# Performance work log

Measured on AMD Instinct MI355X. Metric: run time of the kernel, lower is better.

## Reference

```python
import jax, jax.numpy as jnp
import numpy as np

E, H, G = 1024, 16, 1          # embed_dim, num_heads, gqa_factor
HKV = H // G                   # kv heads
D = E // H                     # head_dim
EKV = HKV * D                  # kv_embed_dim
B, TQ, TK = 4, 512, 1024
CLAMP = float(-np.log(1.0 / 0.98 - 1.0))  # neg_prob_to_phi(clamp_prob=0.98)
SCALE = float(1.0 / np.sqrt(D))           # 1/norm_fact
NEG = -1e30                                # ~ -inf in log space


def monotonic_attention(phi):
    """Log-space monotonic alignment DP over the last axis.
    phi: (N, Ti, Tj) clamped transition logits. Returns log alignment probs, same shape.
    alpha[i,0] = 0 if i==0 else -inf
    alpha[i,j] = logaddexp(alpha[i,j-1] + logsigmoid(phi[i,j-1]),      # stay at row i
                           alpha[i-1,j-1] + logsigmoid(-phi[i-1,j-1])) # advance to row i
    """
    log_p = jax.nn.log_sigmoid(phi)
    log_1mp = jax.nn.log_sigmoid(-phi)
    N, Ti, Tj = phi.shape
    alpha0 = jnp.full((N, Ti), NEG, phi.dtype).at[:, 0].set(0.0)
    neg_col = jnp.full((N, 1), NEG, phi.dtype)

    def step(alpha, cols):
        lp, l1mp = cols  # each (N, Ti)
        stay = alpha + lp
        move = jnp.concatenate([neg_col, (alpha + l1mp)[:, :-1]], axis=1)
        new = jnp.logaddexp(stay, move)
        return new, new

    xs = (jnp.moveaxis(log_p[:, :, :-1], -1, 0), jnp.moveaxis(log_1mp[:, :, :-1], -1, 0))
    _, rest = jax.lax.scan(step, alpha0, xs)             # (Tj-1, N, Ti)
    alphas = jnp.concatenate([alpha0[None], rest], axis=0)  # (Tj, N, Ti)
    return jnp.moveaxis(alphas, 0, -1)                   # (N, Ti, Tj)


def setup_inputs() -> dict:
    k = jax.random.key(0)
    ks = jax.random.split(k, 5)
    bw = float(np.sqrt(6.0 / ((2 * E + 2 * EKV) + E)))  # xavier_uniform bound
    bo = float(1.0 / np.sqrt(E))                        # nn.Linear default bound
    return {
        "query": jax.random.normal(ks[0], (B, TQ, E), jnp.float32),
        "key": jax.random.normal(ks[1], (B, TK, E), jnp.float32),
        "value": jax.random.normal(ks[2], (B, TK, E), jnp.float32),
        "in_proj_weight": jax.random.uniform(ks[3], (2 * E + 2 * EKV, E), jnp.float32, -bw, bw),
        "in_proj_bias": jnp.zeros((2 * E + 2 * EKV,), jnp.float32),
        "out_w": jax.random.uniform(ks[4], (E, E), jnp.float32, -bo, bo),
        "out_b": jnp.zeros((E,), jnp.float32),
    }


def reference(query, key, value, in_proj_weight, in_proj_bias, out_w, out_b):
    qwa, qw, kw, vw = jnp.split(in_proj_weight, [E, 2 * E, 2 * E + EKV], axis=0)
    qba, qb, kb, vb = jnp.split(in_proj_bias, [E, 2 * E, 2 * E + EKV])

    def proj(x, w, b, g):
        y = x @ w.T + b
        Bx, T, _ = x.shape
        return y.reshape(Bx, T, g, HKV, D).transpose(0, 2, 3, 1, 4)  # (B,g,HKV,T,D)

    xqa = proj(query, qwa, qba, G)  # monotonic query
    xq = proj(query, qw, qb, G)     # regular query
    xk = proj(key, kw, kb, 1)
    xv = proj(value, vw, vb, 1)

    # mode = 'many_keys_one_query': DP grid has key rows, query cols
    phi = jnp.einsum('bghqc,bghkc->bghkq', xqa, xk)
    phi = jnp.tanh(phi) * CLAMP  # soft clamp
    mono = monotonic_attention(phi.reshape(-1, TK, TQ)).reshape(B, G, HKV, TK, TQ)
    mono = jnp.swapaxes(mono, -2, -1)  # (B,G,H,TQ,TK)

    reg = jnp.einsum('bghqc,bghkc->bghqk', xq, xk) * SCALE
    attn = jax.nn.softmax(reg + mono, axis=-1)
    xo = jnp.einsum('bghqk,bghkc->bghqc', attn, xv)
    xo = xo.transpose(0, 3, 1, 2, 4).reshape(B, TQ, E)
    return xo @ out_w.T + out_b
```

## Files before the change

kernel.cpp:

```cpp
#include <hip/hip_runtime.h>
#include <hip/hip_fp16.h>
#include <hip/hip_bf16.h>
#include <math.h>

typedef unsigned short u16;
typedef __attribute__((ext_vector_type(8))) short bf16x8;
typedef __attribute__((ext_vector_type(8))) unsigned short u16x8;
typedef __attribute__((ext_vector_type(4))) unsigned short u16x4;
typedef __attribute__((ext_vector_type(4))) float f32x4;

static constexpr float CLAMPF = 3.8918202981106265f;
static constexpr float SCALEF = 0.125f;
static constexpr float ASCALE = 16384.f;

__device__ __forceinline__ u16 f2bf(float x) {
    __hip_bfloat16 h = __float2bfloat16(x);
    return *reinterpret_cast<u16*>(&h);
}

__global__ __launch_bounds__(256)
void cvt_all_k(const float* __restrict__ q, const float* __restrict__ key,
               const float* __restrict__ val, const float* __restrict__ W,
               const float* __restrict__ ow,
               u16* __restrict__ QBF, u16* __restrict__ KBF,
               u16* __restrict__ VBF, u16* __restrict__ WBF,
               u16* __restrict__ OWBF)
{
    long i = (long)blockIdx.x * 256 + threadIdx.x;
    float4 v;
    u16* dst; long off;
    if (i < 524288) {
        dst = QBF; off = i;
        v = ((const float4*)q)[i];
    } else if (i < 1048576) {
        off = i - 524288;
        long r = off >> 8, c4 = off & 255;
        long b = r >> 9, tok = r & 511;
        dst = KBF;
        v = ((const float4*)key)[(b * 1024 + tok) * 256 + c4];
    } else if (i < 1572864) {
        off = i - 1048576;
        long r = off >> 8, c4 = off & 255;
        long b = r >> 9, tok = r & 511;
        dst = VBF;
        v = ((const float4*)val)[(b * 1024 + tok) * 256 + c4];
    } else if (i < 2621440) {
        dst = WBF; off = i - 1572864;
        v = ((const float4*)W)[off];
    } else if (i < 2883584) {
        dst = OWBF; off = i - 2621440;
        v = ((const float4*)ow)[off];
    } else return;
    u16x4 o; o.x = f2bf(v.x); o.y = f2bf(v.y); o.z = f2bf(v.z); o.w = f2bf(v.w);
    ((u16x4*)dst)[off] = o;
}

template<int TM, int TN, int EPI, bool TRI>
__device__ __forceinline__
void mfma_body(u16* As, u16* Bs, int bx, int by, int bz,
               const u16* __restrict__ Ag, const u16* __restrict__ Bg,
               void* __restrict__ Cg, const float* __restrict__ bias,
               int K, int lda, int ldb, int ldc,
               long sAb, long sAh, long sBb, long sBh, long sCb, long sCh,
               int hdiv)
{
    int b = bz / hdiv, h = bz % hdiv;
    const u16* A = Ag + (long)b * sAb + (long)h * sAh;
    const u16* B = Bg + (long)b * sBb + (long)h * sBh;

    int tid = threadIdx.x;
    int bm = by * TM, bn = bx * TN;

    constexpr int AC = TM / 32;
    constexpr int BC = TN / 32;
    int srow = tid >> 3;
    int scol = (tid & 7) * 8;

    int wid = tid >> 6, lane = tid & 63;
    int wr = wid >> 1, wc = wid & 1;
    constexpr int MI = TM / 32;
    constexpr int NI = TN / 32;
    int arow0 = wr * (TM / 2) + (lane & 15);
    int bcol0 = wc * (TN / 2) + (lane & 15);
    int koff = (lane >> 4) * 8;

    if constexpr (TRI) {
        if (bx > by) {
            __half* C = (__half*)Cg + (long)b * sCb + (long)h * sCh;
            int rb = bm + wr * (TM / 2) + (lane >> 4) * 4;
            int cb = bn + wc * (TN / 2) + (lane & 15);
            __half z16 = __float2half(0.f);
#pragma unroll
            for (int mi = 0; mi < MI; ++mi)
#pragma unroll
                for (int ni = 0; ni < NI; ++ni)
#pragma unroll
                    for (int r = 0; r < 4; ++r)
                        C[(long)(rb + 16 * mi + r) * ldc + cb + 16 * ni] = z16;
            return;
        }
    }

    f32x4 acc[MI][NI];
#pragma unroll
    for (int i = 0; i < MI; ++i)
#pragma unroll
        for (int j = 0; j < NI; ++j) acc[i][j] = (f32x4){0.f, 0.f, 0.f, 0.f};

    for (int kt = 0; kt < K; kt += 64) {
        u16x8 av[AC], bv[BC];
#pragma unroll
        for (int c = 0; c < AC; ++c)
            av[c] = *(const u16x8*)(A + (long)(bm + srow + 32 * c) * lda + kt + scol);
#pragma unroll
        for (int c = 0; c < BC; ++c)
            bv[c] = *(const u16x8*)(B + (long)(bn + srow + 32 * c) * ldb + kt + scol);
        __syncthreads();
#pragma unroll
        for (int c = 0; c < AC; ++c)
            *(u16x8*)&As[(srow + 32 * c) * 64 + scol] = av[c];
#pragma unroll
        for (int c = 0; c < BC; ++c)
            *(u16x8*)&Bs[(srow + 32 * c) * 64 + scol] = bv[c];
        __syncthreads();

#pragma unroll
        for (int ks = 0; ks < 2; ++ks) {
            bf16x8 af[MI], bfr[NI];
#pragma unroll
            for (int mi = 0; mi < MI; ++mi)
                af[mi] = *(const bf16x8*)&As[(arow0 + 16 * mi) * 64 + ks * 32 + koff];
#pragma unroll
            for (int ni = 0; ni < NI; ++ni)
                bfr[ni] = *(const bf16x8*)&Bs[(bcol0 + 16 * ni) * 64 + ks * 32 + koff];
#pragma unroll
            for (int mi = 0; mi < MI; ++mi)
#pragma unroll
                for (int ni = 0; ni < NI; ++ni)
                    acc[mi][ni] = __builtin_amdgcn_mfma_f32_16x16x32_bf16(
                        af[mi], bfr[ni], acc[mi][ni], 0, 0, 0);
        }
    }

    int rbase = bm + wr * (TM / 2) + (lane >> 4) * 4;
    int cbase = bn + wc * (TN / 2) + (lane & 15);
#pragma unroll
    for (int mi = 0; mi < MI; ++mi) {
#pragma unroll
        for (int ni = 0; ni < NI; ++ni) {
            int m0 = rbase + 16 * mi;
            int n = cbase + 16 * ni;
            if constexpr (EPI == 0) {
                u16* C = (u16*)Cg + (long)b * sCb + (long)h * sCh;
                float bvv = bias ? bias[n] : 0.f;
#pragma unroll
                for (int r = 0; r < 4; ++r)
                    C[(long)(m0 + r) * ldc + n] = f2bf(acc[mi][ni][r] + bvv);
            } else if constexpr (EPI == 1) {
                __half* C = (__half*)Cg + (long)b * sCb + (long)h * sCh;
#pragma unroll
                for (int r = 0; r < 4; ++r) {
                    float x = acc[mi][ni][r];
                    float e2 = __expf(2.f * x);
                    float tv = CLAMPF - (2.f * CLAMPF) * __builtin_amdgcn_rcpf(e2 + 1.f);
                    float pv = __builtin_amdgcn_rcpf(1.f + __expf(-tv));
                    C[(long)(m0 + r) * ldc + n] = __float2half(pv);
                }
            } else if constexpr (EPI == 3) {
                float* C = (float*)Cg + (long)b * sCb + (long)h * sCh;
                float bvv = bias[n];
#pragma unroll
                for (int r = 0; r < 4; ++r)
                    C[(long)(m0 + r) * ldc + n] = acc[mi][ni][r] + bvv;
            } else {
                u16* C = (u16*)Cg;
                float bvv = bias[n];
                long vaddr = ((long)(b * 16 + (n >> 6)) * 64 + (n & 63)) * 512 + m0;
                u16x4 pk;
                pk.x = f2bf(acc[mi][ni][0] + bvv);
                pk.y = f2bf(acc[mi][ni][1] + bvv);
                pk.z = f2bf(acc[mi][ni][2] + bvv);
                pk.w = f2bf(acc[mi][ni][3] + bvv);
                *(u16x4*)(C + vaddr) = pk;
            }
        }
    }
}

template<int TM, int TN, int EPI, bool TRI = false>
__global__ __launch_bounds__(256)
void mfma_nt(const u16* __restrict__ Ag, const u16* __restrict__ Bg,
             void* __restrict__ Cg, const float* __restrict__ bias,
             int K, int lda, int ldb, int ldc,
             long sAb, long sAh, long sBb, long sBh, long sCb, long sCh,
             int hdiv)
{
    __shared__ u16 As[TM * 64];
    __shared__ u16 Bs[TN * 64];
    mfma_body<TM, TN, EPI, TRI>(As, Bs, blockIdx.x, blockIdx.y, blockIdx.z,
                                Ag, Bg, Cg, bias, K, lda, ldb, ldc,
                                sAb, sAh, sBb, sBh, sCb, sCh, hdiv);
}

__global__ __launch_bounds__(256)
void proj_qk_k(const u16* __restrict__ QBF, const u16* __restrict__ KBF,
               const u16* __restrict__ WBF, const float* __restrict__ ipb,
               u16* __restrict__ XQAQ, u16* __restrict__ XK)
{
    __shared__ u16 As[128 * 64];
    __shared__ u16 Bs[128 * 64];
    int bid = blockIdx.x;
    if (bid < 128) {
        mfma_body<128, 128, 0, false>(As, Bs, bid & 7, bid >> 3, 0,
            QBF, WBF, XQAQ, ipb, 1024, 1024, 1024, 2048, 0, 0, 0, 0, 0, 0, 1);
    } else {
        int idx = bid - 128;
        mfma_body<128, 128, 0, false>(As, Bs, idx & 7, (idx >> 3) & 3, idx >> 5,
            KBF, WBF + 2097152, XK, ipb + 2048, 1024, 1024, 1024, 1024,
            524288L, 0, 0, 0, 524288L, 0, 1);
    }
}


__global__ __launch_bounds__(64)
void dpA_k(const __half* __restrict__ P, __half* __restrict__ BND)
{
    int g = blockIdx.x;
    int n = blockIdx.y;
    int lane = threadIdx.x;
    const __half* p = P + (long)n * 262144;
    int k0 = lane * 8;

    float band[8][9];
#pragma unroll
    for (int r = 0; r < 8; ++r)
#pragma unroll
        for (int d = 0; d < 9; ++d) band[r][d] = 0.f;

    {
        uint4 pc4 = *(const uint4*)(p + (long)(8 * g) * 512 + k0);
        const __half2* hp = (const __half2*)&pc4;
        float pc[8];
        { float2 t = __half22float2(hp[0]); pc[0] = t.x; pc[1] = t.y; }
        { float2 t = __half22float2(hp[1]); pc[2] = t.x; pc[3] = t.y; }
        { float2 t = __half22float2(hp[2]); pc[4] = t.x; pc[5] = t.y; }
        { float2 t = __half22float2(hp[3]); pc[6] = t.x; pc[7] = t.y; }
        float p7s = __shfl_up(pc[7], 1, 64);
#pragma unroll
        for (int r = 0; r < 8; ++r) band[r][0] = pc[r];
        band[0][1] = (lane == 0) ? 0.f : (1.f - p7s);
#pragma unroll
        for (int r = 1; r < 8; ++r) band[r][1] = 1.f - pc[r - 1];
    }

    for (int s = 1; s < 8; ++s) {
        uint4 pc4 = *(const uint4*)(p + (long)(8 * g + s) * 512 + k0);
        const __half2* hp = (const __half2*)&pc4;
        float pc[8];
        { float2 t = __half22float2(hp[0]); pc[0] = t.x; pc[1] = t.y; }
        { float2 t = __half22float2(hp[1]); pc[2] = t.x; pc[3] = t.y; }
        { float2 t = __half22float2(hp[2]); pc[4] = t.x; pc[5] = t.y; }
        { float2 t = __half22float2(hp[3]); pc[6] = t.x; pc[7] = t.y; }
        float p7s = __shfl_up(pc[7], 1, 64);
        float qm0 = (lane == 0) ? 0.f : (1.f - p7s);
        float qm[8];
        qm[0] = qm0;
#pragma unroll
        for (int r = 1; r < 8; ++r) qm[r] = 1.f - pc[r - 1];
        float prev7[9];
#pragma unroll
        for (int d = 0; d < 9; ++d) {
            float v = __shfl_up(band[7][d], 1, 64);
            prev7[d] = (lane == 0) ? 0.f : v;
        }
#pragma unroll
        for (int r = 7; r >= 1; --r) {
#pragma unroll
            for (int d = 8; d >= 1; --d)
                band[r][d] = fmaf(qm[r], band[r - 1][d - 1], pc[r] * band[r][d]);
            band[r][0] = pc[r] * band[r][0];
        }
#pragma unroll
        for (int d = 8; d >= 1; --d)
            band[0][d] = fmaf(qm0, prev7[d - 1], pc[0] * band[0][d]);
        band[0][0] = pc[0] * band[0][0];
    }

    long gb = (long)(n * 63 + g) * 9 * 512;
#pragma unroll
    for (int d = 0; d < 9; ++d) {
        uint4 st;
        __half2 h0 = __floats2half2_rn(band[0][d], band[1][d]);
        __half2 h1 = __floats2half2_rn(band[2][d], band[3][d]);
        __half2 h2 = __floats2half2_rn(band[4][d], band[5][d]);
        __half2 h3 = __floats2half2_rn(band[6][d], band[7][d]);
        st.x = *(unsigned*)&h0; st.y = *(unsigned*)&h1;
        st.z = *(unsigned*)&h2; st.w = *(unsigned*)&h3;
        *(uint4*)(BND + gb + (long)d * 512 + k0) = st;
    }
}

__global__ __launch_bounds__(256)
void dpB_misc_k(const __half* __restrict__ BND, float* __restrict__ BSTATE,
                const u16* __restrict__ QBF, const u16* __restrict__ VBF,
                const u16* __restrict__ WBF, const float* __restrict__ ipb,
                u16* __restrict__ XQAQ, u16* __restrict__ VT)
{
    __shared__ u16 As[128 * 64];
    __shared__ u16 Bs[128 * 64];
    int bid = blockIdx.x;

    if (bid >= 192) {
        int idx = bid - 192;
        mfma_body<128, 128, 0, false>(As, Bs, 8 + (idx & 7), idx >> 3, 0,
            QBF, WBF, XQAQ, ipb, 1024, 1024, 1024, 2048, 0, 0, 0, 0, 0, 0, 1);
        return;
    }
    if (bid >= 64) {
        int idx = bid - 64;
        mfma_body<128, 128, 4, false>(As, Bs, idx & 7, (idx >> 3) & 3, idx >> 5,
            VBF, WBF + 3145728, VT, ipb + 3072, 1024, 1024, 1024, 0,
            524288L, 0, 0, 0, 0, 0, 1);
        return;
    }

    if (threadIdx.x >= 64) return;
    int n = bid;
    int lane = threadIdx.x;
    int k0 = lane * 8;
    const __half* bnd = BND + (long)n * 63 * 9 * 512;
    float* bst = BSTATE + (long)n * 64 * 512;

    float b[8];
#pragma unroll
    for (int r = 0; r < 8; ++r) b[r] = 0.f;
    if (lane == 0) b[0] = ASCALE;
    {
        float4 v0; v0.x = b[0]; v0.y = b[1]; v0.z = b[2]; v0.w = b[3];
        float4 v1; v1.x = b[4]; v1.y = b[5]; v1.z = b[6]; v1.w = b[7];
        *(float4*)(bst + k0) = v0;
        *(float4*)(bst + k0 + 4) = v1;
    }

    uint4 cur[9], nxt[9];
#pragma unroll
    for (int d = 0; d < 9; ++d)
        cur[d] = *(const uint4*)(bnd + (long)d * 512 + k0);

    for (int g = 0; g < 63; ++g) {
        if (g + 1 < 63) {
#pragma unroll
            for (int d = 0; d < 9; ++d)
                nxt[d] = *(const uint4*)(bnd + ((long)(g + 1) * 9 + d) * 512 + k0);
        }
        float pb[8];
#pragma unroll
        for (int r = 0; r < 8; ++r) {
            float v = __shfl_up(b[r], 1, 64);
            pb[r] = (lane == 0) ? 0.f : v;
        }
        float bn[8];
#pragma unroll
        for (int r = 0; r < 8; ++r) bn[r] = 0.f;
#pragma unroll
        for (int d = 0; d < 9; ++d) {
            const __half2* hp = (const __half2*)&cur[d];
            float f[8];
            { float2 t = __half22float2(hp[0]); f[0] = t.x; f[1] = t.y; }
            { float2 t = __half22float2(hp[1]); f[2] = t.x; f[3] = t.y; }
            { float2 t = __half22float2(hp[2]); f[4] = t.x; f[5] = t.y; }
            { float2 t = __half22float2(hp[3]); f[6] = t.x; f[7] = t.y; }
#pragma unroll
            for (int r = 0; r < 8; ++r) {
                float src = (r - d >= 0) ? b[r - d] : pb[8 + r - d];
                bn[r] = fmaf(f[r], src, bn[r]);
            }
        }
#pragma unroll
        for (int r = 0; r < 8; ++r) b[r] = bn[r];
        {
            float4 v0; v0.x = b[0]; v0.y = b[1]; v0.z = b[2]; v0.w = b[3];
            float4 v1; v1.x = b[4]; v1.y = b[5]; v1.z = b[6]; v1.w = b[7];
            *(float4*)(bst + (long)(g + 1) * 512 + k0) = v0;
            *(float4*)(bst + (long)(g + 1) * 512 + k0 + 4) = v1;
        }
#pragma unroll
        for (int d = 0; d < 9; ++d) cur[d] = nxt[d];
    }
}

#define CSTEP(PC, J) do { \
    const __half2* hp = (const __half2*)&(PC); \
    float pv[8]; \
    { float2 t = __half22float2(hp[0]); pv[0] = t.x; pv[1] = t.y; } \
    { float2 t = __half22float2(hp[1]); pv[2] = t.x; pv[3] = t.y; } \
    { float2 t = __half22float2(hp[2]); pv[4] = t.x; pv[5] = t.y; } \
    { float2 t = __half22float2(hp[3]); pv[6] = t.x; pv[7] = t.y; } \
    float c[8]; \
    _Pragma("unroll") \
    for (int r = 0; r < 8; ++r) c[r] = fmaf(-a[r], pv[r], a[r]); \
    float cp = __shfl_up(c[7], 1, 64); \
    if (lane == 0) cp = 0.f; \
    a[0] = fmaf(a[0], pv[0], cp); \
    _Pragma("unroll") \
    for (int r = 1; r < 8; ++r) a[r] = fmaf(a[r], pv[r], c[r - 1]); \
    uint4 st; \
    { __half2 h0 = __floats2half2_rn(a[0], a[1]), h1 = __floats2half2_rn(a[2], a[3]); \
      st.x = *(unsigned*)&h0; st.y = *(unsigned*)&h1; } \
    { __half2 h2 = __floats2half2_rn(a[4], a[5]), h3 = __floats2half2_rn(a[6], a[7]); \
      st.z = *(unsigned*)&h2; st.w = *(unsigned*)&h3; } \
    *(uint4*)(al + (long)(J) * 512 + k0) = st; \
} while (0)

__global__ __launch_bounds__(64)
void dpC_k(const __half* __restrict__ P, const float* __restrict__ BSTATE,
           __half* __restrict__ AL)
{
    int g = blockIdx.x;
    int n = blockIdx.y;
    int lane = threadIdx.x;
    const __half* p = P + (long)n * 262144;
    __half* al = AL + (long)n * 262144;
    int k0 = lane * 8;
    const float* bst = BSTATE + ((long)n * 64 + g) * 512;

    float a[8];
    {
        float4 v0 = *(const float4*)(bst + k0);
        float4 v1 = *(const float4*)(bst + k0 + 4);
        a[0] = v0.x; a[1] = v0.y; a[2] = v0.z; a[3] = v0.w;
        a[4] = v1.x; a[5] = v1.y; a[6] = v1.z; a[7] = v1.w;
    }
    if (g == 0) {
        uint4 st;
        __half2 h0 = __floats2half2_rn(a[0], a[1]), h1 = __floats2half2_rn(a[2], a[3]);
        __half2 h2 = __floats2half2_rn(a[4], a[5]), h3 = __floats2half2_rn(a[6], a[7]);
        st.x = *(unsigned*)&h0; st.y = *(unsigned*)&h1;
        st.z = *(unsigned*)&h2; st.w = *(unsigned*)&h3;
        *(uint4*)(al + k0) = st;
    }

    int t0 = 8 * g + 1;
    int nt = 511 - 8 * g; if (nt > 8) nt = 8;

    uint4 f0 = *(const uint4*)(p + (long)min(8 * g + 0, 510) * 512 + k0);
    uint4 f1 = *(const uint4*)(p + (long)min(8 * g + 1, 510) * 512 + k0);
    uint4 f2 = *(const uint4*)(p + (long)min(8 * g + 2, 510) * 512 + k0);
    uint4 f3 = *(const uint4*)(p + (long)min(8 * g + 3, 510) * 512 + k0);
    uint4 f4 = *(const uint4*)(p + (long)min(8 * g + 4, 510) * 512 + k0);
    uint4 f5 = *(const uint4*)(p + (long)min(8 * g + 5, 510) * 512 + k0);
    uint4 f6 = *(const uint4*)(p + (long)min(8 * g + 6, 510) * 512 + k0);
    uint4 f7 = *(const uint4*)(p + (long)min(8 * g + 7, 510) * 512 + k0);

    CSTEP(f0, t0 + 0);
    CSTEP(f1, t0 + 1);
    CSTEP(f2, t0 + 2);
    CSTEP(f3, t0 + 3);
    CSTEP(f4, t0 + 4);
    CSTEP(f5, t0 + 5);
    CSTEP(f6, t0 + 6);
    if (nt == 8) CSTEP(f7, t0 + 7);
}

__global__ __launch_bounds__(256, 4)
void fused_attn_k(const u16* __restrict__ XQAQ, const u16* __restrict__ XK,
                  const u16* __restrict__ VT, const __half* __restrict__ AL,
                  u16* __restrict__ XO)
{
    __shared__ u16 wtile[4][2048];
    __shared__ float co[4][16][64];
    __shared__ float cml[4][2][16];

    int n = blockIdx.x; int b = n >> 4, h = n & 15;
    int tid = threadIdx.x, wave = tid >> 6, lane = tid & 63;
    int l15 = lane & 15, l4 = lane >> 4;
    int qg = blockIdx.y * 16;
    u16* wlds = wtile[wave];
    int swz = (l15 & 7) << 3;

    float m = -3.0e38f, lsum = 0.f;
    f32x4 o[4];
#pragma unroll
    for (int df = 0; df < 4; ++df) o[df] = (f32x4){0.f, 0.f, 0.f, 0.f};

    if (wave * 128 < qg + 16) {
        const u16* qbase = XQAQ + (long)(b * 512 + qg + l15) * 2048 + 1024 + h * 64 + l4 * 8;
        bf16x8 qf0 = *(const bf16x8*)(qbase);
        bf16x8 qf1 = *(const bf16x8*)(qbase + 32);

        const u16* kbase = XK + (long)(b * 512 + wave * 128 + l15) * 1024 + h * 64 + l4 * 8;
        const __half* abase = AL + (long)(n * 512 + qg + l15) * 512 + wave * 128 + l4 * 4;
        const u16* vbase = VT + (long)(n * 64 + l15) * 512 + wave * 128 + l4 * 8;

        uint2 areg[8];
#pragma unroll
        for (int kf = 0; kf < 8; ++kf)
            areg[kf] = *(const uint2*)(abase + kf * 16);

        f32x4 s[8];
#pragma unroll
        for (int kf = 0; kf < 8; ++kf) {
            const u16* kb = kbase + (long)(kf * 16) * 1024;
            bf16x8 k0 = *(const bf16x8*)kb;
            bf16x8 k1 = *(const bf16x8*)(kb + 32);
            f32x4 acc = (f32x4){0.f, 0.f, 0.f, 0.f};
            acc = __builtin_amdgcn_mfma_f32_16x16x32_bf16(k0, qf0, acc, 0, 0, 0);
            acc = __builtin_amdgcn_mfma_f32_16x16x32_bf16(k1, qf1, acc, 0, 0, 0);
            s[kf] = acc;
        }

        float mt = -3.0e38f;
#pragma unroll
        for (int kf = 0; kf < 8; ++kf)
            mt = fmaxf(mt, fmaxf(fmaxf(s[kf][0], s[kf][1]), fmaxf(s[kf][2], s[kf][3])));
        mt = fmaxf(mt, __shfl_xor(mt, 16, 64));
        mt = fmaxf(mt, __shfl_xor(mt, 32, 64));
        m = mt;
        float negm = -mt * SCALEF;

#pragma unroll
        for (int kf = 0; kf < 8; ++kf) {
            float2 a01 = __half22float2(*(__half2*)&areg[kf].x);
            float2 a23 = __half22float2(*(__half2*)&areg[kf].y);
            float w0 = a01.x * __expf(fmaf(s[kf][0], SCALEF, negm));
            float w1 = a01.y * __expf(fmaf(s[kf][1], SCALEF, negm));
            float w2 = a23.x * __expf(fmaf(s[kf][2], SCALEF, negm));
            float w3 = a23.y * __expf(fmaf(s[kf][3], SCALEF, negm));
            lsum += (w0 + w1) + (w2 + w3);
            u16x4 wp; wp.x = f2bf(w0); wp.y = f2bf(w1); wp.z = f2bf(w2); wp.w = f2bf(w3);
            *(u16x4*)&wlds[(l15 * 128 + kf * 16 + l4 * 4) ^ swz] = wp;
        }

#pragma unroll
        for (int ks2 = 0; ks2 < 4; ++ks2) {
            bf16x8 wf = *(const bf16x8*)&wlds[(l15 * 128 + ks2 * 32 + l4 * 8) ^ swz];
#pragma unroll
            for (int df = 0; df < 4; ++df) {
                const u16* vb = vbase + (long)(df * 16) * 512 + ks2 * 32;
                bf16x8 vf = *(const bf16x8*)vb;
                o[df] = __builtin_amdgcn_mfma_f32_16x16x32_bf16(wf, vf, o[df], 0, 0, 0);
            }
        }

        lsum += __shfl_xor(lsum, 16, 64);
        lsum += __shfl_xor(lsum, 32, 64);
    }

    if (lane < 16) { cml[wave][0][l15] = m; cml[wave][1][l15] = lsum; }
#pragma unroll
    for (int df = 0; df < 4; ++df)
#pragma unroll
        for (int r = 0; r < 4; ++r)
            co[wave][l4 * 4 + r][df * 16 + l15] = o[df][r];
    __syncthreads();

    int q = tid >> 4, d0 = (tid & 15) * 4;
    float m0 = cml[0][0][q], m1 = cml[1][0][q], m2 = cml[2][0][q], m3 = cml[3][0][q];
    float ms = fmaxf(fmaxf(m0, m1), fmaxf(m2, m3));
    float c0w = __expf((m0 - ms) * SCALEF), c1w = __expf((m1 - ms) * SCALEF);
    float c2w = __expf((m2 - ms) * SCALEF), c3w = __expf((m3 - ms) * SCALEF);
    float lt = c0w * cml[0][1][q] + c1w * cml[1][1][q]
             + c2w * cml[2][1][q] + c3w * cml[3][1][q];
    f32x4 o0 = *(const f32x4*)&co[0][q][d0];
    f32x4 o1 = *(const f32x4*)&co[1][q][d0];
    f32x4 o2 = *(const f32x4*)&co[2][q][d0];
    f32x4 o3 = *(const f32x4*)&co[3][q][d0];
    float inv = __builtin_amdgcn_rcpf(lt);
    u16x4 st;
#pragma unroll
    for (int j = 0; j < 4; ++j)
        st[j] = f2bf((c0w * o0[j] + c1w * o1[j] + c2w * o2[j] + c3w * o3[j]) * inv);
    *(u16x4*)&XO[(long)(b * 512 + qg + q) * 1024 + h * 64 + d0] = st;
}

extern "C" void kernel_launch(void* const* d_in, const int* in_sizes, int n_in,
                              void* d_out, int out_size, void* d_ws, size_t ws_size,
                              hipStream_t stream)
{
    const float* q   = (const float*)d_in[0];
    const float* key = (const float*)d_in[1];
    const float* val = (const float*)d_in[2];
    const float* W   = (const float*)d_in[3];
    const float* ipb = (const float*)d_in[4];
    const float* ow  = (const float*)d_in[5];
    const float* ob  = (const float*)d_in[6];
    float* out = (float*)d_out;
    char* w = (char*)d_ws;

    __half* PSIG   = (__half*)(w);
    u16*    XQAQ   = (u16*)(w + 33554432);
    u16*    XK     = (u16*)(w + 41943040);
    u16*    VT     = (u16*)(w + 46137344);
    u16*    XO     = (u16*)(w + 50331648);
    u16*    OWBF   = (u16*)(w + 54525952);
    u16*    KBF    = (u16*)(w + 56623104);
    u16*    VBF    = (u16*)(w + 60817408);
    u16*    WBF    = (u16*)(w + 65011712);
    float*  BSTATE = (float*)(w + 73400320);
    __half* ALPHA  = (__half*)(w + 81788928);
    __half* BND    = (__half*)(w + 81788928);
    u16*    QBF    = (u16*)(w + 50331648);

    dim3 blk(256);

    cvt_all_k<<<dim3(11264), blk, 0, stream>>>(
        q, key, val, W, ow, QBF, KBF, VBF, WBF, OWBF);

    proj_qk_k<<<dim3(256), blk, 0, stream>>>(QBF, KBF, WBF, ipb, XQAQ, XK);

    mfma_nt<128, 128, 1, true><<<dim3(4, 4, 64), blk, 0, stream>>>(
        XQAQ, XK, PSIG, nullptr, 64, 2048, 1024, 512,
        1048576L, 64, 524288L, 64, 4194304L, 262144L, 16);

    dpA_k<<<dim3(63, 64), dim3(64), 0, stream>>>(PSIG, BND);

    dpB_misc_k<<<dim3(320), blk, 0, stream>>>(
        BND, BSTATE, QBF, VBF, WBF, ipb, XQAQ, VT);

    dpC_k<<<dim3(64, 64), dim3(64), 0, stream>>>(PSIG, BSTATE, ALPHA);

    fused_attn_k<<<dim3(64, 32, 1), blk, 0, stream>>>(XQAQ, XK, VT, ALPHA, XO);

    mfma_nt<128, 128, 3><<<dim3(8, 16, 1), blk, 0, stream>>>(
        XO, OWBF, out, ob, 1024, 1024, 1024, 1024, 0, 0, 0, 0, 0, 0, 1);
}
```

Before: 175.2 us.

## Fuse DP column recompute into attention kernel and move GEMMs into dpA

```diff
diff --git a/kernel.cpp b/kernel.cpp
--- a/kernel.cpp
+++ b/kernel.cpp
@@ -222,12 +222,33 @@
 }
 
 
-__global__ __launch_bounds__(64)
-void dpA_k(const __half* __restrict__ P, __half* __restrict__ BND)
-{
-    int g = blockIdx.x;
-    int n = blockIdx.y;
-    int lane = threadIdx.x;
+__global__ __launch_bounds__(256)
+void dpA_k(const __half* __restrict__ P, __half* __restrict__ BND,
+           const u16* __restrict__ QBF, const u16* __restrict__ VBF,
+           const u16* __restrict__ WBF, const float* __restrict__ ipb,
+           u16* __restrict__ XQAQ, u16* __restrict__ VT)
+{
+    __shared__ u16 As[128 * 64];
+    __shared__ u16 Bs[128 * 64];
+    int bid = blockIdx.x;
+
+    if (bid >= 1136) {
+        int idx = bid - 1136;
+        mfma_body<128, 128, 0, false>(As, Bs, 8 + (idx & 7), idx >> 3, 0,
+            QBF, WBF, XQAQ, ipb, 1024, 1024, 1024, 2048, 0, 0, 0, 0, 0, 0, 1);
+        return;
+    }
+    if (bid >= 1008) {
+        int idx = bid - 1008;
+        mfma_body<128, 128, 4, false>(As, Bs, idx & 7, (idx >> 3) & 3, idx >> 5,
+            VBF, WBF + 3145728, VT, ipb + 3072, 1024, 1024, 1024, 0,
+            524288L, 0, 0, 0, 0, 0, 1);
+        return;
+    }
+
+    int wave = threadIdx.x >> 6, lane = threadIdx.x & 63;
+    int idx = bid * 4 + wave;
+    int g = idx % 63, n = idx / 63;
     const __half* p = P + (long)n * 262144;
     int k0 = lane * 8;
 
@@ -300,32 +321,10 @@
     }
 }
 
-__global__ __launch_bounds__(256)
-void dpB_misc_k(const __half* __restrict__ BND, float* __restrict__ BSTATE,
-                const u16* __restrict__ QBF, const u16* __restrict__ VBF,
-                const u16* __restrict__ WBF, const float* __restrict__ ipb,
-                u16* __restrict__ XQAQ, u16* __restrict__ VT)
-{
-    __shared__ u16 As[128 * 64];
-    __shared__ u16 Bs[128 * 64];
-    int bid = blockIdx.x;
-
-    if (bid >= 192) {
-        int idx = bid - 192;
-        mfma_body<128, 128, 0, false>(As, Bs, 8 + (idx & 7), idx >> 3, 0,
-            QBF, WBF, XQAQ, ipb, 1024, 1024, 1024, 2048, 0, 0, 0, 0, 0, 0, 1);
-        return;
-    }
-    if (bid >= 64) {
-        int idx = bid - 64;
-        mfma_body<128, 128, 4, false>(As, Bs, idx & 7, (idx >> 3) & 3, idx >> 5,
-            VBF, WBF + 3145728, VT, ipb + 3072, 1024, 1024, 1024, 0,
-            524288L, 0, 0, 0, 0, 0, 1);
-        return;
-    }
-
-    if (threadIdx.x >= 64) return;
-    int n = bid;
+__global__ __launch_bounds__(64)
+void dpB_k(const __half* __restrict__ BND, float* __restrict__ BSTATE)
+{
+    int n = blockIdx.x;
     int lane = threadIdx.x;
     int k0 = lane * 8;
     const __half* bnd = BND + (long)n * 63 * 9 * 512;
@@ -342,17 +341,20 @@
         *(float4*)(bst + k0 + 4) = v1;
     }
 
-    uint4 cur[9], nxt[9];
+    uint4 cur[9], nxt[9], nxt2[9];
 #pragma unroll
     for (int d = 0; d < 9; ++d)
         cur[d] = *(const uint4*)(bnd + (long)d * 512 + k0);
+#pragma unroll
+    for (int d = 0; d < 9; ++d)
+        nxt[d] = *(const uint4*)(bnd + ((long)min(1, 62) * 9 + d) * 512 + k0);
 
     for (int g = 0; g < 63; ++g) {
-        if (g + 1 < 63) {
-#pragma unroll
-            for (int d = 0; d < 9; ++d)
-                nxt[d] = *(const uint4*)(bnd + ((long)(g + 1) * 9 + d) * 512 + k0);
-        }
+        int gp = min(g + 2, 62);
+#pragma unroll
+        for (int d = 0; d < 9; ++d)
+            nxt2[d] = *(const uint4*)(bnd + ((long)gp * 9 + d) * 512 + k0);
+
         float pb[8];
 #pragma unroll
         for (int r = 0; r < 8; ++r) {
@@ -385,11 +387,11 @@
             *(float4*)(bst + (long)(g + 1) * 512 + k0 + 4) = v1;
         }
 #pragma unroll
-        for (int d = 0; d < 9; ++d) cur[d] = nxt[d];
-    }
-}
-
-#define CSTEP(PC, J) do { \
+        for (int d = 0; d < 9; ++d) { cur[d] = nxt[d]; nxt[d] = nxt2[d]; }
+    }
+}
+
+#define FSTEP(PC, ROW) do { \
     const __half2* hp = (const __half2*)&(PC); \
     float pv[8]; \
     { float2 t = __half22float2(hp[0]); pv[0] = t.x; pv[1] = t.y; } \
@@ -409,74 +411,67 @@
       st.x = *(unsigned*)&h0; st.y = *(unsigned*)&h1; } \
     { __half2 h2 = __floats2half2_rn(a[4], a[5]), h3 = __floats2half2_rn(a[6], a[7]); \
       st.z = *(unsigned*)&h2; st.w = *(unsigned*)&h3; } \
-    *(uint4*)(al + (long)(J) * 512 + k0) = st; \
+    *(uint4*)&alds[ROW][k0] = st; \
 } while (0)
 
-__global__ __launch_bounds__(64)
-void dpC_k(const __half* __restrict__ P, const float* __restrict__ BSTATE,
-           __half* __restrict__ AL)
-{
-    int g = blockIdx.x;
-    int n = blockIdx.y;
-    int lane = threadIdx.x;
-    const __half* p = P + (long)n * 262144;
-    __half* al = AL + (long)n * 262144;
-    int k0 = lane * 8;
-    const float* bst = BSTATE + ((long)n * 64 + g) * 512;
-
-    float a[8];
-    {
-        float4 v0 = *(const float4*)(bst + k0);
-        float4 v1 = *(const float4*)(bst + k0 + 4);
-        a[0] = v0.x; a[1] = v0.y; a[2] = v0.z; a[3] = v0.w;
-        a[4] = v1.x; a[5] = v1.y; a[6] = v1.z; a[7] = v1.w;
-    }
-    if (g == 0) {
-        uint4 st;
-        __half2 h0 = __floats2half2_rn(a[0], a[1]), h1 = __floats2half2_rn(a[2], a[3]);
-        __half2 h2 = __floats2half2_rn(a[4], a[5]), h3 = __floats2half2_rn(a[6], a[7]);
-        st.x = *(unsigned*)&h0; st.y = *(unsigned*)&h1;
-        st.z = *(unsigned*)&h2; st.w = *(unsigned*)&h3;
-        *(uint4*)(al + k0) = st;
-    }
-
-    int t0 = 8 * g + 1;
-    int nt = 511 - 8 * g; if (nt > 8) nt = 8;
-
-    uint4 f0 = *(const uint4*)(p + (long)min(8 * g + 0, 510) * 512 + k0);
-    uint4 f1 = *(const uint4*)(p + (long)min(8 * g + 1, 510) * 512 + k0);
-    uint4 f2 = *(const uint4*)(p + (long)min(8 * g + 2, 510) * 512 + k0);
-    uint4 f3 = *(const uint4*)(p + (long)min(8 * g + 3, 510) * 512 + k0);
-    uint4 f4 = *(const uint4*)(p + (long)min(8 * g + 4, 510) * 512 + k0);
-    uint4 f5 = *(const uint4*)(p + (long)min(8 * g + 5, 510) * 512 + k0);
-    uint4 f6 = *(const uint4*)(p + (long)min(8 * g + 6, 510) * 512 + k0);
-    uint4 f7 = *(const uint4*)(p + (long)min(8 * g + 7, 510) * 512 + k0);
-
-    CSTEP(f0, t0 + 0);
-    CSTEP(f1, t0 + 1);
-    CSTEP(f2, t0 + 2);
-    CSTEP(f3, t0 + 3);
-    CSTEP(f4, t0 + 4);
-    CSTEP(f5, t0 + 5);
-    CSTEP(f6, t0 + 6);
-    if (nt == 8) CSTEP(f7, t0 + 7);
-}
-
-__global__ __launch_bounds__(256, 4)
+__global__ __launch_bounds__(256)
 void fused_attn_k(const u16* __restrict__ XQAQ, const u16* __restrict__ XK,
-                  const u16* __restrict__ VT, const __half* __restrict__ AL,
-                  u16* __restrict__ XO)
+                  const u16* __restrict__ VT, const __half* __restrict__ P,
+                  const float* __restrict__ BSTATE, u16* __restrict__ XO)
 {
     __shared__ u16 wtile[4][2048];
     __shared__ float co[4][16][64];
     __shared__ float cml[4][2][16];
+    __shared__ __half alds[16][520];
 
     int n = blockIdx.x; int b = n >> 4, h = n & 15;
     int tid = threadIdx.x, wave = tid >> 6, lane = tid & 63;
     int l15 = lane & 15, l4 = lane >> 4;
-    int qg = blockIdx.y * 16;
+    int y = blockIdx.y;
+    int qg = y * 16;
     u16* wlds = wtile[wave];
     int swz = (l15 & 7) << 3;
+
+    if (wave == 0) {
+        int k0 = lane * 8;
+        const float* bst = BSTATE + ((long)n * 64 + 2 * y) * 512;
+        const __half* p = P + (long)n * 262144;
+        float a[8];
+        {
+            float4 v0 = *(const float4*)(bst + k0);
+            float4 v1 = *(const float4*)(bst + k0 + 4);
+            a[0] = v0.x; a[1] = v0.y; a[2] = v0.z; a[3] = v0.w;
+            a[4] = v1.x; a[5] = v1.y; a[6] = v1.z; a[7] = v1.w;
+        }
+        {
+            uint4 st;
+            __half2 h0 = __floats2half2_rn(a[0], a[1]), h1 = __floats2half2_rn(a[2], a[3]);
+            __half2 h2 = __floats2half2_rn(a[4], a[5]), h3 = __floats2half2_rn(a[6], a[7]);
+            st.x = *(unsigned*)&h0; st.y = *(unsigned*)&h1;
+            st.z = *(unsigned*)&h2; st.w = *(unsigned*)&h3;
+            *(uint4*)&alds[0][k0] = st;
+        }
+        uint4 f0 = *(const uint4*)(p + (long)(qg + 0) * 512 + k0);
+        uint4 f1 = *(const uint4*)(p + (long)(qg + 1) * 512 + k0);
+        uint4 f2 = *(const uint4*)(p + (long)(qg + 2) * 512 + k0);
+        uint4 f3 = *(const uint4*)(p + (long)(qg + 3) * 512 + k0);
+        uint4 f4 = *(const uint4*)(p + (long)(qg + 4) * 512 + k0);
+        uint4 f5 = *(const uint4*)(p + (long)(qg + 5) * 512 + k0);
+        uint4 f6 = *(const uint4*)(p + (long)(qg + 6) * 512 + k0);
+        uint4 f7 = *(const uint4*)(p + (long)(qg + 7) * 512 + k0);
+        uint4 f8 = *(const uint4*)(p + (long)(qg + 8) * 512 + k0);
+        uint4 f9 = *(const uint4*)(p + (long)(qg + 9) * 512 + k0);
+        uint4 fA = *(const uint4*)(p + (long)(qg + 10) * 512 + k0);
+        uint4 fB = *(const uint4*)(p + (long)(qg + 11) * 512 + k0);
+        uint4 fC = *(const uint4*)(p + (long)(qg + 12) * 512 + k0);
+        uint4 fD = *(const uint4*)(p + (long)(qg + 13) * 512 + k0);
+        uint4 fE = *(const uint4*)(p + (long)(qg + 14) * 512 + k0);
+        FSTEP(f0, 1);  FSTEP(f1, 2);  FSTEP(f2, 3);  FSTEP(f3, 4);
+        FSTEP(f4, 5);  FSTEP(f5, 6);  FSTEP(f6, 7);  FSTEP(f7, 8);
+        FSTEP(f8, 9);  FSTEP(f9, 10); FSTEP(fA, 11); FSTEP(fB, 12);
+        FSTEP(fC, 13); FSTEP(fD, 14); FSTEP(fE, 15);
+    }
+    __syncthreads();
 
     float m = -3.0e38f, lsum = 0.f;
     f32x4 o[4];
@@ -489,13 +484,12 @@
         bf16x8 qf1 = *(const bf16x8*)(qbase + 32);
 
         const u16* kbase = XK + (long)(b * 512 + wave * 128 + l15) * 1024 + h * 64 + l4 * 8;
-        const __half* abase = AL + (long)(n * 512 + qg + l15) * 512 + wave * 128 + l4 * 4;
         const u16* vbase = VT + (long)(n * 64 + l15) * 512 + wave * 128 + l4 * 8;
 
         uint2 areg[8];
 #pragma unroll
         for (int kf = 0; kf < 8; ++kf)
-            areg[kf] = *(const uint2*)(abase + kf * 16);
+            areg[kf] = *(const uint2*)&alds[l15][wave * 128 + kf * 16 + l4 * 4];
 
         f32x4 s[8];
 #pragma unroll
@@ -597,7 +591,6 @@
     u16*    VBF    = (u16*)(w + 60817408);
     u16*    WBF    = (u16*)(w + 65011712);
     float*  BSTATE = (float*)(w + 73400320);
-    __half* ALPHA  = (__half*)(w + 81788928);
     __half* BND    = (__half*)(w + 81788928);
     u16*    QBF    = (u16*)(w + 50331648);
 
@@ -612,14 +605,13 @@
         XQAQ, XK, PSIG, nullptr, 64, 2048, 1024, 512,
         1048576L, 64, 524288L, 64, 4194304L, 262144L, 16);
 
-    dpA_k<<<dim3(63, 64), dim3(64), 0, stream>>>(PSIG, BND);
-
-    dpB_misc_k<<<dim3(320), blk, 0, stream>>>(
-        BND, BSTATE, QBF, VBF, WBF, ipb, XQAQ, VT);
-
-    dpC_k<<<dim3(64, 64), dim3(64), 0, stream>>>(PSIG, BSTATE, ALPHA);
-
-    fused_attn_k<<<dim3(64, 32, 1), blk, 0, stream>>>(XQAQ, XK, VT, ALPHA, XO);
+    dpA_k<<<dim3(1264), blk, 0, stream>>>(
+        PSIG, BND, QBF, VBF, WBF, ipb, XQAQ, VT);
+
+    dpB_k<<<dim3(64), dim3(64), 0, stream>>>(BND, BSTATE);
+
+    fused_attn_k<<<dim3(64, 32, 1), blk, 0, stream>>>(
+        XQAQ, XK, VT, PSIG, BSTATE, XO);
 
     mfma_nt<128, 128, 3><<<dim3(8, 16, 1), blk, 0, stream>>>(
         XO, OWBF, out, ob, 1024, 1024, 1024, 1024, 0, 0, 0, 0, 0, 0, 1);
```

Measured after the change: 183.3 us. 1.05x slower.
